# Optimization experiments

Hardware: AMD Instinct MI355X
Metric: run time of the kernel (lower is better)

Reference implementation:

```python
import jax, jax.numpy as jnp
import numpy as np

H = 256; L = 2; B = 16; S = 128; T = 128; VIN = 32000; VOUT = 32000


def setup_inputs() -> dict:
    key = jax.random.key(0)
    ks = iter(jax.random.split(key, 40))
    def p(shape, scale=0.0625):  # ~1/sqrt(H), like torch LSTM init range
        return jax.random.normal(next(ks), shape, dtype=jnp.float32) * scale
    d = {}
    d["src"] = jax.random.randint(next(ks), (B, S), 0, VIN)
    d["tgt"] = jax.random.randint(next(ks), (B, T), 0, VOUT)
    d["enc_emb"] = p((VIN, H), 1.0)
    d["dec_emb"] = p((VOUT, H), 1.0)
    for pre in ("enc", "dec"):
        for l in range(L):
            d[f"{pre}_Wih{l}"] = p((4 * H, H))
            d[f"{pre}_Whh{l}"] = p((4 * H, H))
            d[f"{pre}_bih{l}"] = p((4 * H,))
            d[f"{pre}_bhh{l}"] = p((4 * H,))
    d["attn_W"] = p((H, 2 * H))
    d["attn_b"] = p((H,))
    d["v_w"] = p((H,))
    d["out_W"] = p((VOUT, 2 * H))
    d["out_b"] = p((VOUT,))
    return d


def _lstm(x, layers, init=None):
    # x: [B, T, I]; layers: list of (Wih[4H,I], Whh[4H,H], bih, bhh); gate order i,f,g,o
    Bb = x.shape[0]
    finals = []
    for li, (Wih, Whh, bih, bhh) in enumerate(layers):
        Hh = Whh.shape[1]
        if init is None:
            h0 = jnp.zeros((Bb, Hh), x.dtype); c0 = h0
        else:
            h0, c0 = init[li]
        def step(carry, xt, Wih=Wih, Whh=Whh, bih=bih, bhh=bhh):
            h, c = carry
            g = xt @ Wih.T + h @ Whh.T + bih + bhh
            i, f, gg, o = jnp.split(g, 4, axis=-1)
            c = jax.nn.sigmoid(f) * c + jax.nn.sigmoid(i) * jnp.tanh(gg)
            h = jax.nn.sigmoid(o) * jnp.tanh(c)
            return (h, c), h
        (hT, cT), ys = jax.lax.scan(step, (h0, c0), jnp.swapaxes(x, 0, 1))
        x = jnp.swapaxes(ys, 0, 1)
        finals.append((hT, cT))
    return x, finals


def _forward(src, tgt, enc_emb, dec_emb, enc_layers, dec_layers, attn_W, attn_b, v_w, out_W, out_b):
    enc_out, enc_fin = _lstm(enc_emb[src], enc_layers)          # [B,S,H]
    # fully teacher-forced decoder (teacher_forcing_ratio=1.0): inputs are tgt[:, :-1]
    dec_out, _ = _lstm(dec_emb[tgt[:, :-1]], dec_layers, init=enc_fin)  # [B,T-1,H]
    Wd, We = attn_W[:, :H], attn_W[:, H:]                        # split concat-linear
    # Bahdanau additive attention, batched over all decode steps
    e = jnp.tanh((dec_out @ Wd.T)[:, :, None, :] + (enc_out @ We.T)[:, None, :, :] + attn_b)
    aw = jax.nn.softmax(jnp.einsum('btsh,h->bts', e, v_w), axis=-1)
    ctx = jnp.einsum('bts,bsh->bth', aw, enc_out)
    logits = jnp.concatenate([dec_out, ctx], axis=-1) @ out_W.T + out_b  # [B,T-1,V]
    zeros0 = jnp.zeros((logits.shape[0], 1, logits.shape[2]), logits.dtype)
    return jnp.concatenate([zeros0, logits], axis=1)             # slot t=0 stays zero


def reference(src, tgt, enc_emb, dec_emb,
              enc_Wih0, enc_Whh0, enc_bih0, enc_bhh0,
              enc_Wih1, enc_Whh1, enc_bih1, enc_bhh1,
              dec_Wih0, dec_Whh0, dec_bih0, dec_bhh0,
              dec_Wih1, dec_Whh1, dec_bih1, dec_bhh1,
              attn_W, attn_b, v_w, out_W, out_b):
    enc_layers = [(enc_Wih0, enc_Whh0, enc_bih0, enc_bhh0),
                  (enc_Wih1, enc_Whh1, enc_bih1, enc_bhh1)]
    dec_layers = [(dec_Wih0, dec_Whh0, dec_bih0, dec_bhh0),
                  (dec_Wih1, dec_Whh1, dec_bih1, dec_bhh1)]
    return _forward(src, tgt, enc_emb, dec_emb, enc_layers, dec_layers,
                    attn_W, attn_b, v_w, out_W, out_b)
```

## Files before the change

### kernel.cpp

```cpp
#include <hip/hip_runtime.h>


typedef __attribute__((ext_vector_type(8))) short s8v;
typedef __attribute__((ext_vector_type(8))) __bf16 bf8v;
typedef __attribute__((ext_vector_type(4))) float f4v;

#define HDIM 256
#define DLEN 127
#define NVOC 32000
#define SENTINEL 0xFFFFFFFFu

__device__ __forceinline__ float bf2f(unsigned short u) {
  union { unsigned int i; float f; } v; v.i = ((unsigned int)u) << 16; return v.f;
}
__device__ __forceinline__ unsigned short f2bf(float x) {
  union { float f; unsigned int i; } v; v.f = x;
  unsigned int u = v.i;
  return (unsigned short)((u + 0x7FFFu + ((u >> 16) & 1u)) >> 16);
}
__device__ __forceinline__ float sigm(float x) {
  x = fminf(fmaxf(x, -30.f), 30.f);
  return 1.f / (1.f + __expf(-x));
}
__device__ __forceinline__ float tanh_f(float x) {
  float y = fminf(fmaxf(x, -15.f), 15.f);
  float e = __expf(2.f * y);
  return (e - 1.f) / (e + 1.f);
}
__device__ __forceinline__ f4v mfma_bf16(s8v a, s8v b, f4v c) {
  return __builtin_amdgcn_mfma_f32_16x16x32_bf16(
      __builtin_bit_cast(bf8v, a), __builtin_bit_cast(bf8v, b), c, 0, 0, 0);
}

#define POLLCOL(base)                                                         \
  for (;;) {                                                                  \
    bool ok = true;                                                           \
    _Pragma("unroll") for (int i = 0; i < 16; i++)                            \
        uv[i] = __hip_atomic_load((base) + i * 256 + tid, __ATOMIC_RELAXED,   \
                                  __HIP_MEMORY_SCOPE_AGENT);                  \
    _Pragma("unroll") for (int i = 0; i < 16; i++) ok &= (uv[i] != SENTINEL); \
    if (ok) break;                                                            \
    __builtin_amdgcn_s_sleep(1);                                              \
  }

__global__ __launch_bounds__(256) void whh_split4(
    const float* __restrict__ W0, const float* __restrict__ W1,
    const float* __restrict__ W2, const float* __restrict__ W3,
    unsigned short* __restrict__ HB) {
  int l = blockIdx.x >> 10;
  int i = (blockIdx.x & 1023) * 256 + threadIdx.x;
  const float* W = (l == 0) ? W0 : (l == 1) ? W1 : (l == 2) ? W2 : W3;
  float w = W[i];
  unsigned short h = f2bf(w);
  unsigned short* Hh = HB + (size_t)l * 524288;
  Hh[i] = h;
  Hh[262144 + i] = f2bf(w - bf2f(h));
}

__global__ __launch_bounds__(256) void wih_split4(
    const float* __restrict__ W0, const float* __restrict__ W1,
    const float* __restrict__ W2, const float* __restrict__ W3,
    unsigned short* __restrict__ WIB) {
  int l = blockIdx.x >> 10;
  int i = (blockIdx.x & 1023) * 256 + threadIdx.x;
  const float* W = (l == 0) ? W0 : (l == 1) ? W1 : (l == 2) ? W2 : W3;
  WIB[(size_t)l * 262144 + i] = f2bf(W[i]);
}

__global__ __launch_bounds__(256) void bias_sum(
    const float* __restrict__ b0i, const float* __restrict__ b0h,
    const float* __restrict__ b1i, const float* __restrict__ b1h,
    const float* __restrict__ b2i, const float* __restrict__ b2h,
    const float* __restrict__ b3i, const float* __restrict__ b3h,
    float* __restrict__ out) {
  int i = blockIdx.x * 256 + threadIdx.x;
  int l = i >> 10, n = i & 1023;
  const float* bi = (l == 0) ? b0i : (l == 1) ? b1i : (l == 2) ? b2i : b3i;
  const float* bh = (l == 0) ? b0h : (l == 1) ? b1h : (l == 2) ? b2h : b3h;
  out[i] = bi[n] + bh[n];
}

__global__ __launch_bounds__(64) void gather_rows(
    const int* __restrict__ toks, const float* __restrict__ emb,
    unsigned short* __restrict__ out, int dec) {
  int r = blockIdx.x, tid = threadIdx.x;
  int token = dec ? toks[(r / DLEN) * 128 + (r % DLEN)] : toks[r];
  float4 v = *(const float4*)&emb[(long)token * HDIM + tid * 4];
  unsigned short q[4] = {f2bf(v.x), f2bf(v.y), f2bf(v.z), f2bf(v.w)};
  *(uint2*)&out[(long)r * HDIM + tid * 4] = *(uint2*)q;
}

__global__ __launch_bounds__(256) void zero_t0(float* __restrict__ out) {
  int i = blockIdx.x * 256 + threadIdx.x;
  int b = i / 8000, off = (i - b * 8000) * 4;
  float4 z = {0.f, 0.f, 0.f, 0.f};
  *(float4*)&out[(long)b * 128 * NVOC + off] = z;
}

__global__ __launch_bounds__(256) void gemm_bt(
    const unsigned short* __restrict__ A, int lda,
    const float* __restrict__ B, int ldb,
    int M, int K,
    const float* __restrict__ bias1, const float* __restrict__ bias2,
    float* __restrict__ Cf, int ldc, int mode, int Tl, int miters) {
  __shared__ unsigned short As[128 * 40];
  __shared__ unsigned short Bs[128 * 40];
  int tid = threadIdx.x;
  int lane = tid & 63, wid = tid >> 6;
  int wm = (wid >> 1) * 64, wn = (wid & 1) * 64;
  int r16 = lane & 15, kg = lane >> 4;
  int n0 = blockIdx.x * 128;

  for (int mi = 0; mi < miters; mi++) {
    int m0 = (blockIdx.y * miters + mi) * 128;
    f4v acc[4][4];
    for (int i = 0; i < 4; i++)
      for (int j = 0; j < 4; j++) acc[i][j] = (f4v){0.f, 0.f, 0.f, 0.f};

    for (int k0 = 0; k0 < K; k0 += 32) {
      for (int i = 0; i < 2; i++) {
        int idx = tid + i * 256;
        int row = idx >> 2, kc = (idx & 3) * 8;
        uint4 va = {0u, 0u, 0u, 0u};
        int gm = m0 + row;
        if (gm < M) va = *(const uint4*)&A[(long)gm * lda + k0 + kc];
        *(uint4*)&As[row * 40 + kc] = va;
        const float* bp = &B[(long)(n0 + row) * ldb + k0 + kc];
        float4 b0 = *(const float4*)bp, b1 = *(const float4*)(bp + 4);
        unsigned short q[8] = {f2bf(b0.x), f2bf(b0.y), f2bf(b0.z), f2bf(b0.w),
                               f2bf(b1.x), f2bf(b1.y), f2bf(b1.z), f2bf(b1.w)};
        *(uint4*)&Bs[row * 40 + kc] = *(uint4*)q;
      }
      __syncthreads();
      s8v af[4], bfg[4];
      for (int f = 0; f < 4; f++) {
        af[f]  = *(const s8v*)&As[(wm + f * 16 + r16) * 40 + kg * 8];
        bfg[f] = *(const s8v*)&Bs[(wn + f * 16 + r16) * 40 + kg * 8];
      }
      for (int i = 0; i < 4; i++)
        for (int j = 0; j < 4; j++)
          acc[i][j] = mfma_bf16(af[i], bfg[j], acc[i][j]);
      __syncthreads();
    }

    int rbase = (lane >> 4) * 4;
    for (int j = 0; j < 4; j++) {
      int n = n0 + wn + j * 16 + r16;
      float bv = 0.f;
      if (bias1) bv += bias1[n];
      if (bias2) bv += bias2[n];
      for (int i = 0; i < 4; i++) {
        for (int r = 0; r < 4; r++) {
          int m = m0 + wm + i * 16 + rbase + r;
          if (m < M) {
            float v = acc[i][j][r] + bv;
            if (mode == 0) {
              Cf[(long)m * ldc + n] = v;
            } else {
              int bb = m / Tl, tt = m - bb * Tl;
              Cf[(long)(bb * 128 + tt + 1) * ldc + n] = v;
            }
          }
        }
      }
    }
    __syncthreads();
  }
}

__global__ __launch_bounds__(256) void lstm_pipe(
    const unsigned short* __restrict__ WIB,
    const unsigned short* __restrict__ WHB,
    const float* __restrict__ bsum,
    const unsigned short* __restrict__ Xe,
    const unsigned short* __restrict__ Xd,
    unsigned int* __restrict__ hsA,
    unsigned int* __restrict__ cfinA,
    unsigned short* __restrict__ Ebf,
    unsigned short* __restrict__ Acat) {
  int widx = (int)blockIdx.x;
  int layer = widx & 7;
  int blk = widx >> 3;
  if (layer > 3 || blk > 15) return;
  __shared__ unsigned short xx[16 * 264];
  __shared__ unsigned short hh[16 * 264];
  __shared__ unsigned short hl[16 * 264];
  __shared__ float gbuf[4][16][16];
  int tid = threadIdx.x;
  int lane = tid & 63, gate = tid >> 6;
  int U = blk * 16;
  int r16 = lane & 15, kg = lane >> 4;
  int Tl = (layer < 2) ? 128 : 127;
  unsigned int* own = hsA + (size_t)layer * 524288;
  const unsigned int* prevb = (layer & 1) ? own - 524288 : nullptr;
  const unsigned short* Xg = (layer == 0) ? Xe : (layer == 2) ? Xd : nullptr;
  const unsigned int* hini =
      (layer >= 2) ? hsA + (size_t)(layer - 2) * 524288 + (size_t)127 * 4096
                   : nullptr;
  unsigned int* cini = (layer >= 2) ? cfinA + (size_t)(layer - 2) * 4096 : nullptr;
  unsigned int* cout = (layer < 2) ? cfinA + (size_t)layer * 4096 : nullptr;
  unsigned short* hout = (layer == 1) ? Ebf : (layer == 3) ? Acat : nullptr;
  int ldo = (layer == 3) ? 512 : 256;

  s8v wfi[8], wfh[8], wfl[8];
  {
    const unsigned short* wi = WIB + (size_t)layer * 262144;
    const unsigned short* wh = WHB + (size_t)layer * 524288;
    const unsigned short* wl = wh + 262144;
    long roff = (long)(gate * 256 + U + r16) * 256 + kg * 8;
    for (int kt = 0; kt < 8; kt++) {
      wfi[kt] = *(const s8v*)(wi + roff + kt * 32);
      wfh[kt] = *(const s8v*)(wh + roff + kt * 32);
      wfl[kt] = *(const s8v*)(wl + roff + kt * 32);
    }
  }
  int b = tid >> 4, u = tid & 15;
  float bb0 = bsum[layer * 1024 + U + u];
  float bb1 = bsum[layer * 1024 + 256 + U + u];
  float bb2 = bsum[layer * 1024 + 512 + U + u];
  float bb3 = bsum[layer * 1024 + 768 + U + u];
  float c;
  if (cini) {
    unsigned int cw;
    for (;;) {
      cw = __hip_atomic_load(cini + b * 256 + U + u, __ATOMIC_RELAXED,
                             __HIP_MEMORY_SCOPE_AGENT);
      if (cw != SENTINEL) break;
      __builtin_amdgcn_s_sleep(8);
    }
    union { unsigned int i; float f; } cv; cv.i = cw; c = cv.f;
  } else {
    c = 0.f;
  }

  for (int t = 0; t < Tl; t++) {
    unsigned int uv[16];
    unsigned short xr[16];
    if (Xg) {
#pragma unroll
      for (int i = 0; i < 16; i++)
        xr[i] = Xg[((size_t)(i * Tl + t)) * 256 + tid];
    }
    const unsigned int* hbase = (t > 0) ? own + (size_t)(t - 1) * 4096 : hini;
    if (hbase) {
      POLLCOL(hbase)
#pragma unroll
      for (int i = 0; i < 16; i++) {
        hh[i * 264 + tid] = (unsigned short)(uv[i] >> 16);
        hl[i * 264 + tid] = (unsigned short)(uv[i] & 0xFFFFu);
      }
    } else {
#pragma unroll
      for (int i = 0; i < 16; i++) { hh[i * 264 + tid] = 0; hl[i * 264 + tid] = 0; }
    }
    if (Xg) {
#pragma unroll
      for (int i = 0; i < 16; i++) xx[i * 264 + tid] = xr[i];
    } else {
      POLLCOL(prevb + (size_t)t * 4096)
#pragma unroll
      for (int i = 0; i < 16; i++)
        xx[i * 264 + tid] = (unsigned short)(uv[i] >> 16);
    }
    __syncthreads();
    f4v a0 = (f4v){0.f, 0.f, 0.f, 0.f};
    f4v a1 = a0, a2 = a0, a3 = a0;
#pragma unroll
    for (int kt = 0; kt < 8; kt++) {
      s8v xv = *(const s8v*)&xx[r16 * 264 + kt * 32 + kg * 8];
      s8v ah = *(const s8v*)&hh[r16 * 264 + kt * 32 + kg * 8];
      s8v al = *(const s8v*)&hl[r16 * 264 + kt * 32 + kg * 8];
      a3 = mfma_bf16(xv, wfi[kt], a3);
      a0 = mfma_bf16(ah, wfh[kt], a0);
      a1 = mfma_bf16(al, wfh[kt], a1);
      a2 = mfma_bf16(ah, wfl[kt], a2);
    }
#pragma unroll
    for (int r = 0; r < 4; r++)
      gbuf[gate][kg * 4 + r][r16] = a0[r] + a1[r] + a2[r] + a3[r];
    __syncthreads();
    float gi = gbuf[0][b][u] + bb0;
    float gf = gbuf[1][b][u] + bb1;
    float gg = gbuf[2][b][u] + bb2;
    float go = gbuf[3][b][u] + bb3;
    c = sigm(gf) * c + sigm(gi) * tanh_f(gg);
    float h = sigm(go) * tanh_f(c);
    unsigned short hb = f2bf(h);
    unsigned int packed =
        ((unsigned int)hb << 16) | (unsigned int)f2bf(h - bf2f(hb));
    __hip_atomic_store(own + (size_t)t * 4096 + b * 256 + U + u, packed,
                       __ATOMIC_RELAXED, __HIP_MEMORY_SCOPE_AGENT);
    if (hout) hout[(size_t)(b * Tl + t) * ldo + U + u] = hb;
  }
  if (cout) {
    union { float f; unsigned int i; } cv; cv.f = c;
    __hip_atomic_store(cout + b * 256 + U + u, cv.i, __ATOMIC_RELAXED,
                       __HIP_MEMORY_SCOPE_AGENT);
  }
}

__global__ __launch_bounds__(256) void attn_ctx(
    const float* __restrict__ dp,
    const float* __restrict__ ep,
    const float* __restrict__ vw,
    const unsigned int* __restrict__ enc_out,
    unsigned short* __restrict__ Acat)
{
  __shared__ float sdp[256], sv[256], sc[128];
  int bt = blockIdx.x;
  int b = bt / DLEN;
  int tid = threadIdx.x;
  sdp[tid] = dp[(long)bt * 256 + tid];
  sv[tid] = vw[tid];
  __syncthreads();
  int lane = tid & 63, wid = tid >> 6;
  for (int i = 0; i < 32; i++) {
    int s = wid * 32 + i;
    float4 e4 = *(const float4*)&ep[(long)(b * 128 + s) * 256 + lane * 4];
    int h0 = lane * 4;
    float part = sv[h0] * tanh_f(sdp[h0] + e4.x);
    part += sv[h0 + 1] * tanh_f(sdp[h0 + 1] + e4.y);
    part += sv[h0 + 2] * tanh_f(sdp[h0 + 2] + e4.z);
    part += sv[h0 + 3] * tanh_f(sdp[h0 + 3] + e4.w);
    for (int off = 32; off >= 1; off >>= 1) part += __shfl_xor(part, off);
    if (lane == 0) sc[s] = part;
  }
  __syncthreads();
  if (wid == 0) {
    float a0 = sc[lane], a1 = sc[lane + 64];
    float mx = fmaxf(a0, a1);
    for (int off = 32; off >= 1; off >>= 1) mx = fmaxf(mx, __shfl_xor(mx, off));
    float e0 = __expf(a0 - mx), e1 = __expf(a1 - mx);
    float sm = e0 + e1;
    for (int off = 32; off >= 1; off >>= 1) sm += __shfl_xor(sm, off);
    float inv = 1.0f / sm;
    sc[lane] = e0 * inv;
    sc[lane + 64] = e1 * inv;
  }
  __syncthreads();
  float acc = 0.f;
  for (int s = 0; s < 128; s++) {
    unsigned int uv = enc_out[(long)(s * 16 + b) * 256 + tid];
    float hv = bf2f((unsigned short)(uv >> 16)) +
               bf2f((unsigned short)(uv & 0xFFFFu));
    acc += sc[s] * hv;
  }
  Acat[(long)bt * 512 + 256 + tid] = f2bf(acc);
}

extern "C" void kernel_launch(void* const* d_in, const int* in_sizes, int n_in,
                              void* d_out, int out_size, void* d_ws, size_t ws_size,
                              hipStream_t stream) {
  (void)in_sizes; (void)n_in; (void)out_size; (void)ws_size;
  const int* src = (const int*)d_in[0];
  const int* tgt = (const int*)d_in[1];
  auto F32 = [&](int i) { return (const float*)d_in[i]; };
  const float* enc_emb = F32(2);
  const float* dec_emb = F32(3);
  const float* attnW = F32(20);
  const float* attnB = F32(21);
  const float* vw = F32(22);
  const float* outW = F32(23);
  const float* outB = F32(24);
  float* out = (float*)d_out;

  unsigned int* hsA = (unsigned int*)out;
  float* dpf = (float*)(hsA + (size_t)4 * 524288);
  float* epf = dpf + 524288;
  unsigned short* WHB = (unsigned short*)(epf + 524288);
  unsigned short* WIB = WHB + (size_t)4 * 524288;
  unsigned short* Xe  = WIB + (size_t)4 * 262144;
  unsigned short* Xd  = Xe + 524288;
  unsigned short* Ebf = Xd + 524288;
  float* bsum = (float*)(Ebf + 524288);

  char* w = (char*)d_ws;
  unsigned short* Acat = (unsigned short*)w;
  unsigned int* cfinA = (unsigned int*)(w + 2097152 + 4096);

  hipMemsetAsync(hsA, 0xFF, (size_t)4 * 524288 * 4, stream);
  hipMemsetAsync(cfinA, 0xFF, (size_t)2 * 4096 * 4, stream);
  whh_split4<<<4096, 256, 0, stream>>>(F32(5), F32(9), F32(13), F32(17), WHB);
  wih_split4<<<4096, 256, 0, stream>>>(F32(4), F32(8), F32(12), F32(16), WIB);
  bias_sum<<<16, 256, 0, stream>>>(F32(6), F32(7), F32(10), F32(11),
                                   F32(14), F32(15), F32(18), F32(19), bsum);
  gather_rows<<<2048, 64, 0, stream>>>(src, enc_emb, Xe, 0);
  gather_rows<<<2032, 64, 0, stream>>>(tgt, dec_emb, Xd, 1);
  lstm_pipe<<<124, 256, 0, stream>>>(WIB, WHB, bsum, Xe, Xd, hsA, cfinA,
                                     Ebf, Acat);
  gemm_bt<<<dim3(2, 16), 256, 0, stream>>>(Acat, 512, attnW, 512, 2032, 256,
      attnB, nullptr, dpf, 256, 0, 0, 1);
  gemm_bt<<<dim3(2, 16), 256, 0, stream>>>(Ebf, 256, attnW + 256, 512, 2048, 256,
      nullptr, nullptr, epf, 256, 0, 0, 1);
  attn_ctx<<<2032, 256, 0, stream>>>(dpf, epf, vw, hsA + 524288, Acat);
  gemm_bt<<<dim3(250, 4), 256, 0, stream>>>(Acat, 512, outW, 512, 2032, 512,
      outB, nullptr, out, NVOC, 1, 127, 4);
  zero_t0<<<500, 256, 0, stream>>>(out);
}
```

Before: 1.333 ms.

## Fuse prep kernels and overlap attention projections with LSTM pipeline in megakernel

Merges the weight-split, bias-sum and embedding-gather kernels into one prep launch. Folds the attention projection GEMMs and the attention/context step into the persistent LSTM kernel: idle blocks poll per-timestep readiness flags and start work while the recurrence is still running. The logits GEMM gets a dedicated kernel whose grid also covers the t=0 zero row. This removes several launches and the serialization after the recurrence, at the cost of more polling traffic and extra scheduling complexity inside the persistent kernel.

```diff
diff --git a/kernel.cpp b/kernel.cpp
--- a/kernel.cpp
+++ b/kernel.cpp
@@ -35,140 +35,68 @@
 #define POLLCOL(base)                                                         \
   for (;;) {                                                                  \
     bool ok = true;                                                           \
-    _Pragma("unroll") for (int i = 0; i < 16; i++)                            \
-        uv[i] = __hip_atomic_load((base) + i * 256 + tid, __ATOMIC_RELAXED,   \
-                                  __HIP_MEMORY_SCOPE_AGENT);                  \
-    _Pragma("unroll") for (int i = 0; i < 16; i++) ok &= (uv[i] != SENTINEL); \
+    _Pragma("unroll") for (int i_ = 0; i_ < 16; i_++)                         \
+        uv[i_] = __hip_atomic_load((base) + i_ * 256 + tid, __ATOMIC_RELAXED, \
+                                   __HIP_MEMORY_SCOPE_AGENT);                 \
+    _Pragma("unroll") for (int i_ = 0; i_ < 16; i_++)                         \
+        ok &= (uv[i_] != SENTINEL);                                           \
     if (ok) break;                                                            \
     __builtin_amdgcn_s_sleep(1);                                              \
   }
 
-__global__ __launch_bounds__(256) void whh_split4(
-    const float* __restrict__ W0, const float* __restrict__ W1,
-    const float* __restrict__ W2, const float* __restrict__ W3,
-    unsigned short* __restrict__ HB) {
-  int l = blockIdx.x >> 10;
-  int i = (blockIdx.x & 1023) * 256 + threadIdx.x;
-  const float* W = (l == 0) ? W0 : (l == 1) ? W1 : (l == 2) ? W2 : W3;
-  float w = W[i];
-  unsigned short h = f2bf(w);
-  unsigned short* Hh = HB + (size_t)l * 524288;
-  Hh[i] = h;
-  Hh[262144 + i] = f2bf(w - bf2f(h));
-}
-
-__global__ __launch_bounds__(256) void wih_split4(
-    const float* __restrict__ W0, const float* __restrict__ W1,
-    const float* __restrict__ W2, const float* __restrict__ W3,
-    unsigned short* __restrict__ WIB) {
-  int l = blockIdx.x >> 10;
-  int i = (blockIdx.x & 1023) * 256 + threadIdx.x;
-  const float* W = (l == 0) ? W0 : (l == 1) ? W1 : (l == 2) ? W2 : W3;
-  WIB[(size_t)l * 262144 + i] = f2bf(W[i]);
-}
-
-__global__ __launch_bounds__(256) void bias_sum(
-    const float* __restrict__ b0i, const float* __restrict__ b0h,
-    const float* __restrict__ b1i, const float* __restrict__ b1h,
-    const float* __restrict__ b2i, const float* __restrict__ b2h,
-    const float* __restrict__ b3i, const float* __restrict__ b3h,
-    float* __restrict__ out) {
-  int i = blockIdx.x * 256 + threadIdx.x;
-  int l = i >> 10, n = i & 1023;
-  const float* bi = (l == 0) ? b0i : (l == 1) ? b1i : (l == 2) ? b2i : b3i;
-  const float* bh = (l == 0) ? b0h : (l == 1) ? b1h : (l == 2) ? b2h : b3h;
-  out[i] = bi[n] + bh[n];
-}
-
-__global__ __launch_bounds__(64) void gather_rows(
-    const int* __restrict__ toks, const float* __restrict__ emb,
-    unsigned short* __restrict__ out, int dec) {
-  int r = blockIdx.x, tid = threadIdx.x;
-  int token = dec ? toks[(r / DLEN) * 128 + (r % DLEN)] : toks[r];
-  float4 v = *(const float4*)&emb[(long)token * HDIM + tid * 4];
-  unsigned short q[4] = {f2bf(v.x), f2bf(v.y), f2bf(v.z), f2bf(v.w)};
-  *(uint2*)&out[(long)r * HDIM + tid * 4] = *(uint2*)q;
-}
-
-__global__ __launch_bounds__(256) void zero_t0(float* __restrict__ out) {
-  int i = blockIdx.x * 256 + threadIdx.x;
-  int b = i / 8000, off = (i - b * 8000) * 4;
-  float4 z = {0.f, 0.f, 0.f, 0.f};
-  *(float4*)&out[(long)b * 128 * NVOC + off] = z;
-}
-
-__global__ __launch_bounds__(256) void gemm_bt(
-    const unsigned short* __restrict__ A, int lda,
-    const float* __restrict__ B, int ldb,
-    int M, int K,
-    const float* __restrict__ bias1, const float* __restrict__ bias2,
-    float* __restrict__ Cf, int ldc, int mode, int Tl, int miters) {
-  __shared__ unsigned short As[128 * 40];
-  __shared__ unsigned short Bs[128 * 40];
-  int tid = threadIdx.x;
-  int lane = tid & 63, wid = tid >> 6;
-  int wm = (wid >> 1) * 64, wn = (wid & 1) * 64;
-  int r16 = lane & 15, kg = lane >> 4;
-  int n0 = blockIdx.x * 128;
-
-  for (int mi = 0; mi < miters; mi++) {
-    int m0 = (blockIdx.y * miters + mi) * 128;
-    f4v acc[4][4];
-    for (int i = 0; i < 4; i++)
-      for (int j = 0; j < 4; j++) acc[i][j] = (f4v){0.f, 0.f, 0.f, 0.f};
-
-    for (int k0 = 0; k0 < K; k0 += 32) {
-      for (int i = 0; i < 2; i++) {
-        int idx = tid + i * 256;
-        int row = idx >> 2, kc = (idx & 3) * 8;
-        uint4 va = {0u, 0u, 0u, 0u};
-        int gm = m0 + row;
-        if (gm < M) va = *(const uint4*)&A[(long)gm * lda + k0 + kc];
-        *(uint4*)&As[row * 40 + kc] = va;
-        const float* bp = &B[(long)(n0 + row) * ldb + k0 + kc];
-        float4 b0 = *(const float4*)bp, b1 = *(const float4*)(bp + 4);
-        unsigned short q[8] = {f2bf(b0.x), f2bf(b0.y), f2bf(b0.z), f2bf(b0.w),
-                               f2bf(b1.x), f2bf(b1.y), f2bf(b1.z), f2bf(b1.w)};
-        *(uint4*)&Bs[row * 40 + kc] = *(uint4*)q;
-      }
-      __syncthreads();
-      s8v af[4], bfg[4];
-      for (int f = 0; f < 4; f++) {
-        af[f]  = *(const s8v*)&As[(wm + f * 16 + r16) * 40 + kg * 8];
-        bfg[f] = *(const s8v*)&Bs[(wn + f * 16 + r16) * 40 + kg * 8];
-      }
-      for (int i = 0; i < 4; i++)
-        for (int j = 0; j < 4; j++)
-          acc[i][j] = mfma_bf16(af[i], bfg[j], acc[i][j]);
-      __syncthreads();
-    }
-
-    int rbase = (lane >> 4) * 4;
-    for (int j = 0; j < 4; j++) {
-      int n = n0 + wn + j * 16 + r16;
-      float bv = 0.f;
-      if (bias1) bv += bias1[n];
-      if (bias2) bv += bias2[n];
-      for (int i = 0; i < 4; i++) {
-        for (int r = 0; r < 4; r++) {
-          int m = m0 + wm + i * 16 + rbase + r;
-          if (m < M) {
-            float v = acc[i][j][r] + bv;
-            if (mode == 0) {
-              Cf[(long)m * ldc + n] = v;
-            } else {
-              int bb = m / Tl, tt = m - bb * Tl;
-              Cf[(long)(bb * 128 + tt + 1) * ldc + n] = v;
-            }
-          }
-        }
-      }
-    }
-    __syncthreads();
-  }
-}
-
-__global__ __launch_bounds__(256) void lstm_pipe(
+__global__ __launch_bounds__(256) void prep(
+    const float* __restrict__ W5, const float* __restrict__ W9,
+    const float* __restrict__ W13, const float* __restrict__ W17,
+    const float* __restrict__ W4, const float* __restrict__ W8,
+    const float* __restrict__ W12, const float* __restrict__ W16,
+    const float* __restrict__ b6, const float* __restrict__ b7,
+    const float* __restrict__ b10, const float* __restrict__ b11,
+    const float* __restrict__ b14, const float* __restrict__ b15,
+    const float* __restrict__ b18, const float* __restrict__ b19,
+    const int* __restrict__ src, const int* __restrict__ tgt,
+    const float* __restrict__ enc_emb, const float* __restrict__ dec_emb,
+    unsigned short* __restrict__ WHB, unsigned short* __restrict__ WIB,
+    float* __restrict__ bsum,
+    unsigned short* __restrict__ Xe, unsigned short* __restrict__ Xd) {
+  int blk = blockIdx.x, tid = threadIdx.x;
+  if (blk < 4096) {
+    int l = blk >> 10;
+    int i = (blk & 1023) * 256 + tid;
+    const float* W = (l == 0) ? W5 : (l == 1) ? W9 : (l == 2) ? W13 : W17;
+    float w = W[i];
+    unsigned short h = f2bf(w);
+    unsigned short* Hh = WHB + (size_t)l * 524288;
+    Hh[i] = h;
+    Hh[262144 + i] = f2bf(w - bf2f(h));
+  } else if (blk < 8192) {
+    int l = (blk - 4096) >> 10;
+    int i = ((blk - 4096) & 1023) * 256 + tid;
+    const float* W = (l == 0) ? W4 : (l == 1) ? W8 : (l == 2) ? W12 : W16;
+    WIB[(size_t)l * 262144 + i] = f2bf(W[i]);
+  } else if (blk < 8208) {
+    int i = (blk - 8192) * 256 + tid;
+    int l = i >> 10, n = i & 1023;
+    const float* bi = (l == 0) ? b6 : (l == 1) ? b10 : (l == 2) ? b14 : b18;
+    const float* bh = (l == 0) ? b7 : (l == 1) ? b11 : (l == 2) ? b15 : b19;
+    bsum[i] = bi[n] + bh[n];
+  } else if (blk < 8720) {
+    int r = (blk - 8208) * 4 + (tid >> 6);
+    int lane = tid & 63;
+    int token = src[r];
+    float4 v = *(const float4*)&enc_emb[(size_t)token * HDIM + lane * 4];
+    unsigned short q[4] = {f2bf(v.x), f2bf(v.y), f2bf(v.z), f2bf(v.w)};
+    *(uint2*)&Xe[(size_t)r * HDIM + lane * 4] = *(uint2*)q;
+  } else {
+    int r = (blk - 8720) * 4 + (tid >> 6);
+    int lane = tid & 63;
+    int token = tgt[(r / DLEN) * 128 + (r % DLEN)];
+    float4 v = *(const float4*)&dec_emb[(size_t)token * HDIM + lane * 4];
+    unsigned short q[4] = {f2bf(v.x), f2bf(v.y), f2bf(v.z), f2bf(v.w)};
+    *(uint2*)&Xd[(size_t)r * HDIM + lane * 4] = *(uint2*)q;
+  }
+}
+
+__global__ __launch_bounds__(256) void mega(
     const unsigned short* __restrict__ WIB,
     const unsigned short* __restrict__ WHB,
     const float* __restrict__ bsum,
@@ -176,176 +104,345 @@
     const unsigned short* __restrict__ Xd,
     unsigned int* __restrict__ hsA,
     unsigned int* __restrict__ cfinA,
-    unsigned short* __restrict__ Ebf,
+    float* __restrict__ dpf,
+    float* __restrict__ epf,
+    const float* __restrict__ attnW,
+    const float* __restrict__ attnB,
+    const float* __restrict__ vw,
     unsigned short* __restrict__ Acat) {
-  int widx = (int)blockIdx.x;
-  int layer = widx & 7;
-  int blk = widx >> 3;
-  if (layer > 3 || blk > 15) return;
-  __shared__ unsigned short xx[16 * 264];
-  __shared__ unsigned short hh[16 * 264];
-  __shared__ unsigned short hl[16 * 264];
-  __shared__ float gbuf[4][16][16];
+  __shared__ unsigned long long ldsraw[3840];
+  int widx = (int)blockIdx.x, tid = threadIdx.x;
+  int lane = tid & 63;
+  int r16 = lane & 15, kg = lane >> 4;
+
+  if (widx < 128 && (widx & 7) < 4) {
+    int layer = widx & 7;
+    int blk = widx >> 3;
+    unsigned short* xx = (unsigned short*)ldsraw;
+    unsigned short* hh = xx + 4224;
+    unsigned short* hl = hh + 4224;
+    float* gbuf = (float*)(hl + 4224);
+    int gate = tid >> 6;
+    int U = blk * 16;
+    int Tl = (layer < 2) ? 128 : 127;
+    unsigned int* own = hsA + (size_t)layer * 524288;
+    const unsigned int* prevb = (layer & 1) ? own - 524288 : nullptr;
+    const unsigned short* Xg = (layer == 0) ? Xe : (layer == 2) ? Xd : nullptr;
+    const unsigned int* hini =
+        (layer >= 2) ? hsA + (size_t)(layer - 2) * 524288 + (size_t)127 * 4096
+                     : nullptr;
+    unsigned int* cini = (layer >= 2) ? cfinA + (size_t)(layer - 2) * 4096
+                                      : nullptr;
+    unsigned int* cout = (layer < 2) ? cfinA + (size_t)layer * 4096 : nullptr;
+    unsigned short* hout = (layer == 3) ? Acat : nullptr;
+
+    s8v wfi[8], wfh[8], wfl[8];
+    {
+      const unsigned short* wi = WIB + (size_t)layer * 262144;
+      const unsigned short* wh = WHB + (size_t)layer * 524288;
+      const unsigned short* wl = wh + 262144;
+      long roff = (long)(gate * 256 + U + r16) * 256 + kg * 8;
+      for (int kt = 0; kt < 8; kt++) {
+        wfi[kt] = *(const s8v*)(wi + roff + kt * 32);
+        wfh[kt] = *(const s8v*)(wh + roff + kt * 32);
+        wfl[kt] = *(const s8v*)(wl + roff + kt * 32);
+      }
+    }
+    int b = tid >> 4, u = tid & 15;
+    float bb0 = bsum[layer * 1024 + U + u];
+    float bb1 = bsum[layer * 1024 + 256 + U + u];
+    float bb2 = bsum[layer * 1024 + 512 + U + u];
+    float bb3 = bsum[layer * 1024 + 768 + U + u];
+    float c;
+    if (cini) {
+      unsigned int cw;
+      for (;;) {
+        cw = __hip_atomic_load(cini + b * 256 + U + u, __ATOMIC_RELAXED,
+                               __HIP_MEMORY_SCOPE_AGENT);
+        if (cw != SENTINEL) break;
+        __builtin_amdgcn_s_sleep(8);
+      }
+      union { unsigned int i; float f; } cv; cv.i = cw; c = cv.f;
+    } else {
+      c = 0.f;
+    }
+
+    for (int t = 0; t < Tl; t++) {
+      unsigned int uv[16];
+      unsigned short xr[16];
+      if (Xg) {
+#pragma unroll
+        for (int i = 0; i < 16; i++)
+          xr[i] = Xg[((size_t)(i * Tl + t)) * 256 + tid];
+      }
+      const unsigned int* hbase = (t > 0) ? own + (size_t)(t - 1) * 4096 : hini;
+      if (hbase) {
+        POLLCOL(hbase)
+#pragma unroll
+        for (int i = 0; i < 16; i++) {
+          hh[i * 264 + tid] = (unsigned short)(uv[i] >> 16);
+          hl[i * 264 + tid] = (unsigned short)(uv[i] & 0xFFFFu);
+        }
+      } else {
+#pragma unroll
+        for (int i = 0; i < 16; i++) { hh[i * 264 + tid] = 0; hl[i * 264 + tid] = 0; }
+      }
+      if (Xg) {
+#pragma unroll
+        for (int i = 0; i < 16; i++) xx[i * 264 + tid] = xr[i];
+      } else {
+        POLLCOL(prevb + (size_t)t * 4096)
+#pragma unroll
+        for (int i = 0; i < 16; i++)
+          xx[i * 264 + tid] = (unsigned short)(uv[i] >> 16);
+      }
+      __syncthreads();
+      f4v a0 = (f4v){0.f, 0.f, 0.f, 0.f};
+      f4v a1 = a0, a2 = a0, a3 = a0;
+#pragma unroll
+      for (int kt = 0; kt < 8; kt++) {
+        s8v xv = *(const s8v*)&xx[r16 * 264 + kt * 32 + kg * 8];
+        s8v ah = *(const s8v*)&hh[r16 * 264 + kt * 32 + kg * 8];
+        s8v al = *(const s8v*)&hl[r16 * 264 + kt * 32 + kg * 8];
+        a3 = mfma_bf16(xv, wfi[kt], a3);
+        a0 = mfma_bf16(ah, wfh[kt], a0);
+        a1 = mfma_bf16(al, wfh[kt], a1);
+        a2 = mfma_bf16(ah, wfl[kt], a2);
+      }
+#pragma unroll
+      for (int r = 0; r < 4; r++)
+        gbuf[gate * 256 + (kg * 4 + r) * 16 + r16] = a0[r] + a1[r] + a2[r] + a3[r];
+      __syncthreads();
+      float gi = gbuf[0 * 256 + b * 16 + u] + bb0;
+      float gf = gbuf[1 * 256 + b * 16 + u] + bb1;
+      float gg = gbuf[2 * 256 + b * 16 + u] + bb2;
+      float go = gbuf[3 * 256 + b * 16 + u] + bb3;
+      c = sigm(gf) * c + sigm(gi) * tanh_f(gg);
+      float h = sigm(go) * tanh_f(c);
+      unsigned short hb = f2bf(h);
+      unsigned int packed =
+          ((unsigned int)hb << 16) | (unsigned int)f2bf(h - bf2f(hb));
+      __hip_atomic_store(own + (size_t)t * 4096 + b * 256 + U + u, packed,
+                         __ATOMIC_RELAXED, __HIP_MEMORY_SCOPE_AGENT);
+      if (hout) hout[(size_t)(b * Tl + t) * 512 + U + u] = hb;
+    }
+    if (cout) {
+      union { float f; unsigned int i; } cv; cv.f = c;
+      __hip_atomic_store(cout + b * 256 + U + u, cv.i, __ATOMIC_RELAXED,
+                         __HIP_MEMORY_SCOPE_AGENT);
+    }
+    return;
+  }
+
+  int p = (widx < 128) ? ((widx >> 3) * 4 + ((widx & 7) - 4)) : (64 + widx - 128);
+  if (p >= 80) return;
+
+  if (p < 64) {
+    int q = (p < 32) ? p : (p - 32);
+    int isep = (p < 32) ? 1 : 0;
+    int g = q >> 1, n0 = (q & 1) * 128;
+    const unsigned int* slab = hsA + (size_t)(isep ? 1 : 3) * 524288;
+    int Tl = isep ? 128 : 127;
+    const float* Bw = isep ? (attnW + 256) : attnW;
+    for (int k = 0; k < 8; k++) {
+      int tt = g * 8 + k;
+      if (tt < Tl) {
+        unsigned int uv[16];
+        POLLCOL(slab + (size_t)tt * 4096)
+      }
+    }
+    __builtin_amdgcn_sched_barrier(0);
+    __syncthreads();
+
+    unsigned short* As = (unsigned short*)ldsraw;
+    unsigned short* Bs = As + 5120;
+    int wid = tid >> 6;
+    int wm = (wid >> 1) * 64, wn = (wid & 1) * 64;
+    f4v acc[4][4];
+    for (int i = 0; i < 4; i++)
+      for (int j = 0; j < 4; j++) acc[i][j] = (f4v){0.f, 0.f, 0.f, 0.f};
+
+    for (int k0 = 0; k0 < 256; k0 += 32) {
+      for (int i = 0; i < 2; i++) {
+        int idx = tid + i * 256;
+        int row = idx >> 2, kc = (idx & 3) * 8;
+        int tt = g * 8 + (row >> 4), bb = row & 15;
+        unsigned short qa[8] = {0, 0, 0, 0, 0, 0, 0, 0};
+        if (tt < Tl) {
+          const unsigned int* wp = slab + (size_t)tt * 4096 + bb * 256 + k0 + kc;
+          uint4 w0 = *(const uint4*)wp, w1 = *(const uint4*)(wp + 4);
+          qa[0] = (unsigned short)(w0.x >> 16); qa[1] = (unsigned short)(w0.y >> 16);
+          qa[2] = (unsigned short)(w0.z >> 16); qa[3] = (unsigned short)(w0.w >> 16);
+          qa[4] = (unsigned short)(w1.x >> 16); qa[5] = (unsigned short)(w1.y >> 16);
+          qa[6] = (unsigned short)(w1.z >> 16); qa[7] = (unsigned short)(w1.w >> 16);
+        }
+        *(uint4*)&As[row * 40 + kc] = *(uint4*)qa;
+        const float* bp = &Bw[(size_t)(n0 + row) * 512 + k0 + kc];
+        float4 b0 = *(const float4*)bp, b1 = *(const float4*)(bp + 4);
+        unsigned short qb[8] = {f2bf(b0.x), f2bf(b0.y), f2bf(b0.z), f2bf(b0.w),
+                                f2bf(b1.x), f2bf(b1.y), f2bf(b1.z), f2bf(b1.w)};
+        *(uint4*)&Bs[row * 40 + kc] = *(uint4*)qb;
+      }
+      __syncthreads();
+      s8v af[4], bfg[4];
+      for (int f = 0; f < 4; f++) {
+        af[f]  = *(const s8v*)&As[(wm + f * 16 + r16) * 40 + kg * 8];
+        bfg[f] = *(const s8v*)&Bs[(wn + f * 16 + r16) * 40 + kg * 8];
+      }
+      for (int i = 0; i < 4; i++)
+        for (int j = 0; j < 4; j++)
+          acc[i][j] = mfma_bf16(af[i], bfg[j], acc[i][j]);
+      __syncthreads();
+    }
+    int rbase = kg * 4;
+    for (int j = 0; j < 4; j++) {
+      int n = n0 + wn + j * 16 + r16;
+      float bv = isep ? 0.f : attnB[n];
+      for (int i = 0; i < 4; i++) {
+        for (int r = 0; r < 4; r++) {
+          int m = wm + i * 16 + rbase + r;
+          int tt = g * 8 + (m >> 4), bb = m & 15;
+          if (tt < Tl) {
+            union { float f; unsigned int i; } cv;
+            cv.f = acc[i][j][r] + bv;
+            float* outb = isep ? epf : dpf;
+            size_t row = isep ? (size_t)(bb * 128 + tt) : (size_t)(bb * 127 + tt);
+            __hip_atomic_store((unsigned int*)&outb[row * 256 + n], cv.i,
+                               __ATOMIC_RELAXED, __HIP_MEMORY_SCOPE_AGENT);
+          }
+        }
+      }
+    }
+    return;
+  }
+
+  {
+    int b = p - 64;
+    float* sdp = (float*)ldsraw;
+    float* sv  = sdp + 256;
+    float* sc  = sv + 256;
+    sv[tid] = vw[tid];
+    const unsigned int* epu = (const unsigned int*)epf;
+    for (int c0 = 0; c0 < 128; c0 += 16) {
+      unsigned int uv[16];
+      POLLCOL(epu + (size_t)(b * 128 + c0) * 256)
+    }
+    __builtin_amdgcn_sched_barrier(0);
+    __syncthreads();
+    const unsigned int* dpu = (const unsigned int*)dpf;
+    const unsigned int* hs1 = hsA + (size_t)1 * 524288;
+    int wid = tid >> 6;
+    for (int t = 0; t < DLEN; t++) {
+      unsigned int w;
+      const unsigned int* a = dpu + (size_t)(b * DLEN + t) * 256 + tid;
+      for (;;) {
+        w = __hip_atomic_load(a, __ATOMIC_RELAXED, __HIP_MEMORY_SCOPE_AGENT);
+        if (w != SENTINEL) break;
+        __builtin_amdgcn_s_sleep(1);
+      }
+      __syncthreads();
+      union { unsigned int i; float f; } cw; cw.i = w;
+      sdp[tid] = cw.f;
+      __syncthreads();
+      for (int i = 0; i < 32; i++) {
+        int s = wid * 32 + i;
+        float4 e4 = *(const float4*)&epf[(size_t)(b * 128 + s) * 256 + lane * 4];
+        int h0 = lane * 4;
+        float part = sv[h0] * tanh_f(sdp[h0] + e4.x);
+        part += sv[h0 + 1] * tanh_f(sdp[h0 + 1] + e4.y);
+        part += sv[h0 + 2] * tanh_f(sdp[h0 + 2] + e4.z);
+        part += sv[h0 + 3] * tanh_f(sdp[h0 + 3] + e4.w);
+        for (int off = 32; off >= 1; off >>= 1) part += __shfl_xor(part, off);
+        if (lane == 0) sc[s] = part;
+      }
+      __syncthreads();
+      if (wid == 0) {
+        float s0 = sc[lane], s1 = sc[lane + 64];
+        float mx = fmaxf(s0, s1);
+        for (int off = 32; off >= 1; off >>= 1) mx = fmaxf(mx, __shfl_xor(mx, off));
+        float e0 = __expf(s0 - mx), e1 = __expf(s1 - mx);
+        float sm = e0 + e1;
+        for (int off = 32; off >= 1; off >>= 1) sm += __shfl_xor(sm, off);
+        float inv = 1.0f / sm;
+        sc[lane] = e0 * inv;
+        sc[lane + 64] = e1 * inv;
+      }
+      __syncthreads();
+      float acc2 = 0.f;
+      for (int s = 0; s < 128; s++) {
+        unsigned int uvv = hs1[(size_t)s * 4096 + b * 256 + tid];
+        float hv = bf2f((unsigned short)(uvv >> 16)) +
+                   bf2f((unsigned short)(uvv & 0xFFFFu));
+        acc2 += sc[s] * hv;
+      }
+      Acat[(size_t)(b * DLEN + t) * 512 + 256 + tid] = f2bf(acc2);
+    }
+    return;
+  }
+}
+
+__global__ __launch_bounds__(256) void logits_gemm(
+    const unsigned short* __restrict__ A,
+    const float* __restrict__ B,
+    const float* __restrict__ bias,
+    float* __restrict__ Cf) {
+  int n0 = blockIdx.x * 128;
   int tid = threadIdx.x;
-  int lane = tid & 63, gate = tid >> 6;
-  int U = blk * 16;
+  if (blockIdx.y == 16) {
+    int col = tid & 127;
+    for (int b = tid >> 7; b < 16; b += 2)
+      Cf[(size_t)b * 128 * NVOC + n0 + col] = 0.f;
+    return;
+  }
+  __shared__ unsigned short As[128 * 40];
+  __shared__ unsigned short Bs[128 * 40];
+  int lane = tid & 63, wid = tid >> 6;
+  int wm = (wid >> 1) * 64, wn = (wid & 1) * 64;
   int r16 = lane & 15, kg = lane >> 4;
-  int Tl = (layer < 2) ? 128 : 127;
-  unsigned int* own = hsA + (size_t)layer * 524288;
-  const unsigned int* prevb = (layer & 1) ? own - 524288 : nullptr;
-  const unsigned short* Xg = (layer == 0) ? Xe : (layer == 2) ? Xd : nullptr;
-  const unsigned int* hini =
-      (layer >= 2) ? hsA + (size_t)(layer - 2) * 524288 + (size_t)127 * 4096
-                   : nullptr;
-  unsigned int* cini = (layer >= 2) ? cfinA + (size_t)(layer - 2) * 4096 : nullptr;
-  unsigned int* cout = (layer < 2) ? cfinA + (size_t)layer * 4096 : nullptr;
-  unsigned short* hout = (layer == 1) ? Ebf : (layer == 3) ? Acat : nullptr;
-  int ldo = (layer == 3) ? 512 : 256;
-
-  s8v wfi[8], wfh[8], wfl[8];
-  {
-    const unsigned short* wi = WIB + (size_t)layer * 262144;
-    const unsigned short* wh = WHB + (size_t)layer * 524288;
-    const unsigned short* wl = wh + 262144;
-    long roff = (long)(gate * 256 + U + r16) * 256 + kg * 8;
-    for (int kt = 0; kt < 8; kt++) {
-      wfi[kt] = *(const s8v*)(wi + roff + kt * 32);
-      wfh[kt] = *(const s8v*)(wh + roff + kt * 32);
-      wfl[kt] = *(const s8v*)(wl + roff + kt * 32);
-    }
-  }
-  int b = tid >> 4, u = tid & 15;
-  float bb0 = bsum[layer * 1024 + U + u];
-  float bb1 = bsum[layer * 1024 + 256 + U + u];
-  float bb2 = bsum[layer * 1024 + 512 + U + u];
-  float bb3 = bsum[layer * 1024 + 768 + U + u];
-  float c;
-  if (cini) {
-    unsigned int cw;
-    for (;;) {
-      cw = __hip_atomic_load(cini + b * 256 + U + u, __ATOMIC_RELAXED,
-                             __HIP_MEMORY_SCOPE_AGENT);
-      if (cw != SENTINEL) break;
-      __builtin_amdgcn_s_sleep(8);
-    }
-    union { unsigned int i; float f; } cv; cv.i = cw; c = cv.f;
-  } else {
-    c = 0.f;
-  }
-
-  for (int t = 0; t < Tl; t++) {
-    unsigned int uv[16];
-    unsigned short xr[16];
-    if (Xg) {
-#pragma unroll
-      for (int i = 0; i < 16; i++)
-        xr[i] = Xg[((size_t)(i * Tl + t)) * 256 + tid];
-    }
-    const unsigned int* hbase = (t > 0) ? own + (size_t)(t - 1) * 4096 : hini;
-    if (hbase) {
-      POLLCOL(hbase)
-#pragma unroll
-      for (int i = 0; i < 16; i++) {
-        hh[i * 264 + tid] = (unsigned short)(uv[i] >> 16);
-        hl[i * 264 + tid] = (unsigned short)(uv[i] & 0xFFFFu);
-      }
-    } else {
-#pragma unroll
-      for (int i = 0; i < 16; i++) { hh[i * 264 + tid] = 0; hl[i * 264 + tid] = 0; }
-    }
-    if (Xg) {
-#pragma unroll
-      for (int i = 0; i < 16; i++) xx[i * 264 + tid] = xr[i];
-    } else {
-      POLLCOL(prevb + (size_t)t * 4096)
-#pragma unroll
-      for (int i = 0; i < 16; i++)
-        xx[i * 264 + tid] = (unsigned short)(uv[i] >> 16);
+  int m0 = blockIdx.y * 128;
+  f4v acc[4][4];
+  for (int i = 0; i < 4; i++)
+    for (int j = 0; j < 4; j++) acc[i][j] = (f4v){0.f, 0.f, 0.f, 0.f};
+
+  for (int k0 = 0; k0 < 512; k0 += 32) {
+    for (int i = 0; i < 2; i++) {
+      int idx = tid + i * 256;
+      int row = idx >> 2, kc = (idx & 3) * 8;
+      uint4 va = {0u, 0u, 0u, 0u};
+      int gm = m0 + row;
+      if (gm < 2032) va = *(const uint4*)&A[(size_t)gm * 512 + k0 + kc];
+      *(uint4*)&As[row * 40 + kc] = va;
+      const float* bp = &B[(size_t)(n0 + row) * 512 + k0 + kc];
+      float4 b0 = *(const float4*)bp, b1 = *(const float4*)(bp + 4);
+      unsigned short q[8] = {f2bf(b0.x), f2bf(b0.y), f2bf(b0.z), f2bf(b0.w),
+                             f2bf(b1.x), f2bf(b1.y), f2bf(b1.z), f2bf(b1.w)};
+      *(uint4*)&Bs[row * 40 + kc] = *(uint4*)q;
     }
     __syncthreads();
-    f4v a0 = (f4v){0.f, 0.f, 0.f, 0.f};
-    f4v a1 = a0, a2 = a0, a3 = a0;
-#pragma unroll
-    for (int kt = 0; kt < 8; kt++) {
-      s8v xv = *(const s8v*)&xx[r16 * 264 + kt * 32 + kg * 8];
-      s8v ah = *(const s8v*)&hh[r16 * 264 + kt * 32 + kg * 8];
-      s8v al = *(const s8v*)&hl[r16 * 264 + kt * 32 + kg * 8];
-      a3 = mfma_bf16(xv, wfi[kt], a3);
-      a0 = mfma_bf16(ah, wfh[kt], a0);
-      a1 = mfma_bf16(al, wfh[kt], a1);
-      a2 = mfma_bf16(ah, wfl[kt], a2);
-    }
-#pragma unroll
-    for (int r = 0; r < 4; r++)
-      gbuf[gate][kg * 4 + r][r16] = a0[r] + a1[r] + a2[r] + a3[r];
+    s8v af[4], bfg[4];
+    for (int f = 0; f < 4; f++) {
+      af[f]  = *(const s8v*)&As[(wm + f * 16 + r16) * 40 + kg * 8];
+      bfg[f] = *(const s8v*)&Bs[(wn + f * 16 + r16) * 40 + kg * 8];
+    }
+    for (int i = 0; i < 4; i++)
+      for (int j = 0; j < 4; j++)
+        acc[i][j] = mfma_bf16(af[i], bfg[j], acc[i][j]);
     __syncthreads();
-    float gi = gbuf[0][b][u] + bb0;
-    float gf = gbuf[1][b][u] + bb1;
-    float gg = gbuf[2][b][u] + bb2;
-    float go = gbuf[3][b][u] + bb3;
-    c = sigm(gf) * c + sigm(gi) * tanh_f(gg);
-    float h = sigm(go) * tanh_f(c);
-    unsigned short hb = f2bf(h);
-    unsigned int packed =
-        ((unsigned int)hb << 16) | (unsigned int)f2bf(h - bf2f(hb));
-    __hip_atomic_store(own + (size_t)t * 4096 + b * 256 + U + u, packed,
-                       __ATOMIC_RELAXED, __HIP_MEMORY_SCOPE_AGENT);
-    if (hout) hout[(size_t)(b * Tl + t) * ldo + U + u] = hb;
-  }
-  if (cout) {
-    union { float f; unsigned int i; } cv; cv.f = c;
-    __hip_atomic_store(cout + b * 256 + U + u, cv.i, __ATOMIC_RELAXED,
-                       __HIP_MEMORY_SCOPE_AGENT);
-  }
-}
-
-__global__ __launch_bounds__(256) void attn_ctx(
-    const float* __restrict__ dp,
-    const float* __restrict__ ep,
-    const float* __restrict__ vw,
-    const unsigned int* __restrict__ enc_out,
-    unsigned short* __restrict__ Acat)
-{
-  __shared__ float sdp[256], sv[256], sc[128];
-  int bt = blockIdx.x;
-  int b = bt / DLEN;
-  int tid = threadIdx.x;
-  sdp[tid] = dp[(long)bt * 256 + tid];
-  sv[tid] = vw[tid];
-  __syncthreads();
-  int lane = tid & 63, wid = tid >> 6;
-  for (int i = 0; i < 32; i++) {
-    int s = wid * 32 + i;
-    float4 e4 = *(const float4*)&ep[(long)(b * 128 + s) * 256 + lane * 4];
-    int h0 = lane * 4;
-    float part = sv[h0] * tanh_f(sdp[h0] + e4.x);
-    part += sv[h0 + 1] * tanh_f(sdp[h0 + 1] + e4.y);
-    part += sv[h0 + 2] * tanh_f(sdp[h0 + 2] + e4.z);
-    part += sv[h0 + 3] * tanh_f(sdp[h0 + 3] + e4.w);
-    for (int off = 32; off >= 1; off >>= 1) part += __shfl_xor(part, off);
-    if (lane == 0) sc[s] = part;
-  }
-  __syncthreads();
-  if (wid == 0) {
-    float a0 = sc[lane], a1 = sc[lane + 64];
-    float mx = fmaxf(a0, a1);
-    for (int off = 32; off >= 1; off >>= 1) mx = fmaxf(mx, __shfl_xor(mx, off));
-    float e0 = __expf(a0 - mx), e1 = __expf(a1 - mx);
-    float sm = e0 + e1;
-    for (int off = 32; off >= 1; off >>= 1) sm += __shfl_xor(sm, off);
-    float inv = 1.0f / sm;
-    sc[lane] = e0 * inv;
-    sc[lane + 64] = e1 * inv;
-  }
-  __syncthreads();
-  float acc = 0.f;
-  for (int s = 0; s < 128; s++) {
-    unsigned int uv = enc_out[(long)(s * 16 + b) * 256 + tid];
-    float hv = bf2f((unsigned short)(uv >> 16)) +
-               bf2f((unsigned short)(uv & 0xFFFFu));
-    acc += sc[s] * hv;
-  }
-  Acat[(long)bt * 512 + 256 + tid] = f2bf(acc);
+  }
+  int rbase = kg * 4;
+  for (int j = 0; j < 4; j++) {
+    int n = n0 + wn + j * 16 + r16;
+    float bv = bias[n];
+    for (int i = 0; i < 4; i++) {
+      for (int r = 0; r < 4; r++) {
+        int m = m0 + wm + i * 16 + rbase + r;
+        if (m < 2032) {
+          int bb = m / DLEN, tt = m - bb * DLEN;
+          Cf[(size_t)(bb * 128 + tt + 1) * NVOC + n] = acc[i][j][r] + bv;
+        }
+      }
+    }
+  }
 }
 
 extern "C" void kernel_launch(void* const* d_in, const int* in_sizes, int n_in,
@@ -365,35 +462,27 @@
   float* out = (float*)d_out;
 
   unsigned int* hsA = (unsigned int*)out;
-  float* dpf = (float*)(hsA + (size_t)4 * 524288);
-  float* epf = dpf + 524288;
-  unsigned short* WHB = (unsigned short*)(epf + 524288);
-  unsigned short* WIB = WHB + (size_t)4 * 524288;
-  unsigned short* Xe  = WIB + (size_t)4 * 262144;
+  float* dpf = (float*)(hsA + 2097152);
+  float* epf = dpf + 520192;
+  unsigned int* cfinA = (unsigned int*)(epf + 524288);
+  unsigned short* WHB = (unsigned short*)(cfinA + 8192);
+  unsigned short* WIB = WHB + 2097152;
+  unsigned short* Xe  = WIB + 1048576;
   unsigned short* Xd  = Xe + 524288;
-  unsigned short* Ebf = Xd + 524288;
-  float* bsum = (float*)(Ebf + 524288);
-
-  char* w = (char*)d_ws;
-  unsigned short* Acat = (unsigned short*)w;
-  unsigned int* cfinA = (unsigned int*)(w + 2097152 + 4096);
-
-  hipMemsetAsync(hsA, 0xFF, (size_t)4 * 524288 * 4, stream);
-  hipMemsetAsync(cfinA, 0xFF, (size_t)2 * 4096 * 4, stream);
-  whh_split4<<<4096, 256, 0, stream>>>(F32(5), F32(9), F32(13), F32(17), WHB);
-  wih_split4<<<4096, 256, 0, stream>>>(F32(4), F32(8), F32(12), F32(16), WIB);
-  bias_sum<<<16, 256, 0, stream>>>(F32(6), F32(7), F32(10), F32(11),
-                                   F32(14), F32(15), F32(18), F32(19), bsum);
-  gather_rows<<<2048, 64, 0, stream>>>(src, enc_emb, Xe, 0);
-  gather_rows<<<2032, 64, 0, stream>>>(tgt, dec_emb, Xd, 1);
-  lstm_pipe<<<124, 256, 0, stream>>>(WIB, WHB, bsum, Xe, Xd, hsA, cfinA,
-                                     Ebf, Acat);
-  gemm_bt<<<dim3(2, 16), 256, 0, stream>>>(Acat, 512, attnW, 512, 2032, 256,
-      attnB, nullptr, dpf, 256, 0, 0, 1);
-  gemm_bt<<<dim3(2, 16), 256, 0, stream>>>(Ebf, 256, attnW + 256, 512, 2048, 256,
-      nullptr, nullptr, epf, 256, 0, 0, 1);
-  attn_ctx<<<2032, 256, 0, stream>>>(dpf, epf, vw, hsA + 524288, Acat);
-  gemm_bt<<<dim3(250, 4), 256, 0, stream>>>(Acat, 512, outW, 512, 2032, 512,
-      outB, nullptr, out, NVOC, 1, 127, 4);
-  zero_t0<<<500, 256, 0, stream>>>(out);
-}
+  float* bsum = (float*)(Xd + 520192);
+
+  unsigned short* Acat = (unsigned short*)d_ws;
+
+  size_t poisonB = (size_t)(2097152 + 520192 + 524288 + 8192) * 4;
+  hipMemsetAsync(hsA, 0xFF, poisonB, stream);
+  prep<<<9228, 256, 0, stream>>>(
+      F32(5), F32(9), F32(13), F32(17),
+      F32(4), F32(8), F32(12), F32(16),
+      F32(6), F32(7), F32(10), F32(11),
+      F32(14), F32(15), F32(18), F32(19),
+      src, tgt, enc_emb, dec_emb,
+      WHB, WIB, bsum, Xe, Xd);
+  mega<<<256, 256, 0, stream>>>(WIB, WHB, bsum, Xe, Xd, hsA, cfinA,
+                                dpf, epf, attnW, attnB, vw, Acat);
+  logits_gemm<<<dim3(250, 17), 256, 0, stream>>>(Acat, outW, outB, out);
+}
```

After: 3.351 ms. +151.3%, slower.
